# Optimization experiments

Measured on AMD Instinct MI355X. Metric: run time of the kernel, lower is better.

Reference implementation:

```python
import jax, jax.numpy as jnp
import numpy as np

B, IN_DIM, NUM_CLASS, OUT_CAPS, INIT_DIM, PCAP, T, LEAVES = 4096, 100, 4, 16, 64, 32, 16, 32
SUB = OUT_CAPS // NUM_CLASS          # 4
D = IN_DIM + INIT_DIM                # 164, digit_input_dim
M = PCAP + 1                         # 33 primary capsules
VBS = 256                            # GBN virtual batch size
EPS = 1e-5
DIN1 = T * SUB                       # 64, decoder input dim
DIN2 = DIN1 + 16                     # 80, after cat with conv1 out (base_outdim//2)


def entmax15(x, axis=-1):
    # exact alpha=1.5 entmax (Peters/Niculae/Martins), sort-based threshold
    x = jnp.moveaxis(x, axis, -1)
    x = (x - jnp.max(x, axis=-1, keepdims=True)) / 2.0
    d = x.shape[-1]
    xs = -jnp.sort(-x, axis=-1)  # descending
    rho = jnp.arange(1, d + 1, dtype=x.dtype)
    mean = jnp.cumsum(xs, axis=-1) / rho
    mean_sq = jnp.cumsum(xs * xs, axis=-1) / rho
    ss = rho * (mean_sq - mean * mean)
    delta_nz = jnp.clip((1.0 - ss) / rho, 0.0)
    tau = mean - jnp.sqrt(delta_nz)
    support = jnp.sum(tau <= xs, axis=-1, keepdims=True)
    tau_star = jnp.take_along_axis(tau, support - 1, axis=-1)
    out = jnp.clip(x - tau_star, 0.0) ** 2
    return jnp.moveaxis(out, -1, axis)


def layernorm(x, g, b):
    m = jnp.mean(x, axis=-1, keepdims=True)
    v = jnp.mean((x - m) ** 2, axis=-1, keepdims=True)
    return (x - m) / jnp.sqrt(v + EPS) * g + b


def gbn(x, g, b):
    # Ghost BatchNorm (training-mode batch stats per virtual batch of VBS)
    n = x.shape[0] // VBS
    xr = x.reshape(n, VBS, -1)
    m = jnp.mean(xr, axis=1, keepdims=True)
    v = jnp.mean((xr - m) ** 2, axis=1, keepdims=True)
    xr = (xr - m) / jnp.sqrt(v + EPS)
    return (xr * g + b).reshape(x.shape)


def abstract_layer(x, mask_w, fc_w, fc_b, bn_g, bn_b, out_dim):
    # mask_w: [P, Din], fc_w: [P, 2*out, Din] (grouped 1x1 conv), fc_b: [P, 2*out]
    mask = entmax15(mask_w, axis=-1)                      # [P, Din]
    mx = mask[None] * x[:, None, :]                       # [B, P, Din]
    h = jnp.einsum('bpd,pod->bpo', mx, fc_w) + fc_b       # [B, P, 2*out]
    bsz, p = h.shape[0], h.shape[1]
    h = gbn(h.reshape(bsz, -1), bn_g, bn_b).reshape(bsz, p, 2 * out_dim)
    # GLU-style gate per path, summed over paths
    return jnp.sum(jax.nn.relu(jax.nn.sigmoid(h[..., :out_dim]) * h[..., out_dim:]), axis=1)


def forward(x, y, init_w, init_b, enc_ln_g, enc_ln_b, prim_fc, route_w, thread,
            leaves, caps_ln_g, caps_ln_b, m1_w, fc1_w, fc1_b, bn1_g, bn1_b,
            m2_w, fc2_w, fc2_b, bn2_g, bn2_b, dec_w, dec_b):
    bsz = x.shape[0]
    # ---- CapsuleEncoder ----
    init_x = x @ init_w.T + init_b                        # [B, INIT_DIM]
    f = jnp.concatenate([x, init_x], axis=1)              # [B, D]
    caps = f[:, :, None] * prim_fc[None]                  # [B, D, PCAP]
    caps = jnp.concatenate([caps, f[:, :, None]], axis=-1)  # [B, D, M]
    caps = jnp.swapaxes(caps, -1, -2)                     # [B, M, D]
    caps = layernorm(caps, enc_ln_g, enc_ln_b)
    # ---- InferCapsule ----
    w = entmax15(route_w, axis=-2)                        # [M, N, D, T], entmax over D
    priors = jnp.einsum('bmd,mndt->bmnt', caps, w)        # [B, M, N, T]
    lh = leaves / jnp.maximum(jnp.linalg.norm(leaves, axis=-1, keepdims=True), 1e-12)
    votes = jax.nn.sigmoid(jnp.einsum('lt,bmnt->bmnl', lh, priors))  # [B, M, N, L]
    dis = jnp.mean((votes - jnp.mean(votes, axis=1, keepdims=True)) ** 2, axis=-1)  # [B, M, N]
    wgt = jax.nn.relu(thread ** 2 - dis)
    prob = jax.nn.softmax(wgt, axis=-2)                   # softmax over M
    hidden = layernorm(jnp.einsum('bmn,bmnt->bnt', prob, priors), caps_ln_g, caps_ln_b)  # [B, N, T]
    # ---- head (eval: no dropout) ----
    norms = jnp.sqrt(jnp.sum(hidden ** 2, axis=-1))       # [B, N]
    pred = jnp.sum(norms.reshape(bsz, NUM_CLASS, SUB), axis=-1)
    # ---- label-gated capsule selection ----
    yr = jnp.tile(y, (1, SUB)).reshape(bsz, SUB, NUM_CLASS)
    hsel = jnp.sum(hidden.reshape(bsz, SUB, NUM_CLASS, T) * yr[..., None], axis=2)
    hsel = hsel.reshape(bsz, DIN1)                        # [B, 64]
    # ---- decoder: CapsuleDecoder_BasicBlock + Linear ----
    out1 = abstract_layer(hsel, m1_w, fc1_w, fc1_b, bn1_g, bn1_b, 16)
    h2 = jnp.concatenate([hsel, out1], axis=-1)           # [B, 80]
    out2 = abstract_layer(h2, m2_w, fc2_w, fc2_b, bn2_g, bn2_b, 32)
    rec = out2 @ dec_w.T + dec_b                          # [B, IN_DIM]
    return pred, rec


def setup_inputs() -> dict:
    ks = jax.random.split(jax.random.key(0), 20)
    d = {}
    d['x'] = jax.random.normal(ks[0], (B, IN_DIM), jnp.float32)
    d['y'] = jax.nn.one_hot(jax.random.randint(ks[1], (B,), 0, NUM_CLASS), NUM_CLASS, dtype=jnp.float32)
    d['init_w'] = jax.random.normal(ks[2], (INIT_DIM, IN_DIM), jnp.float32) * 0.1
    d['init_b'] = jnp.zeros((INIT_DIM,), jnp.float32)
    d['enc_ln_g'] = jnp.ones((D,), jnp.float32)
    d['enc_ln_b'] = jnp.zeros((D,), jnp.float32)
    d['prim_fc'] = jax.random.normal(ks[3], (D, PCAP), jnp.float32)
    d['route_w'] = jax.random.normal(ks[4], (M, OUT_CAPS, D, T), jnp.float32)
    d['thread'] = jax.random.uniform(ks[5], (1, M, OUT_CAPS), jnp.float32)
    d['leaves'] = jax.random.uniform(ks[6], (LEAVES, T), jnp.float32)
    d['caps_ln_g'] = jnp.ones((T,), jnp.float32)
    d['caps_ln_b'] = jnp.zeros((T,), jnp.float32)
    d['m1_w'] = jax.random.uniform(ks[7], (3, DIN1), jnp.float32)
    d['fc1_w'] = jax.random.normal(ks[8], (3, 32, DIN1), jnp.float32) * 0.1
    d['fc1_b'] = jnp.zeros((3, 32), jnp.float32)
    d['bn1_g'] = jnp.ones((3 * 32,), jnp.float32)
    d['bn1_b'] = jnp.zeros((3 * 32,), jnp.float32)
    d['m2_w'] = jax.random.uniform(ks[9], (3, DIN2), jnp.float32)
    d['fc2_w'] = jax.random.normal(ks[10], (3, 64, DIN2), jnp.float32) * 0.1
    d['fc2_b'] = jnp.zeros((3, 64), jnp.float32)
    d['bn2_g'] = jnp.ones((3 * 64,), jnp.float32)
    d['bn2_b'] = jnp.zeros((3 * 64,), jnp.float32)
    d['dec_w'] = jax.random.normal(ks[11], (IN_DIM, 32), jnp.float32) * 0.1
    d['dec_b'] = jnp.zeros((IN_DIM,), jnp.float32)
    return d


def reference(x, y, init_w, init_b, enc_ln_g, enc_ln_b, prim_fc, route_w, thread,
              leaves, caps_ln_g, caps_ln_b, m1_w, fc1_w, fc1_b, bn1_g, bn1_b,
              m2_w, fc2_w, fc2_b, bn2_g, bn2_b, dec_w, dec_b):
    return forward(x, y, init_w, init_b, enc_ln_g, enc_ln_b, prim_fc, route_w, thread,
                   leaves, caps_ln_g, caps_ln_b, m1_w, fc1_w, fc1_b, bn1_g, bn1_b,
                   m2_w, fc2_w, fc2_b, bn2_g, bn2_b, dec_w, dec_b)
```

## Files before the change

### kernel.cpp

```cpp
#include <hip/hip_runtime.h>
#include <hip/hip_fp16.h>

#define BATCH 4096
#define NCLS  4
#define INDIM 100
#define INITD 64
#define DD    164
#define DDP   192
#define MM    33
#define TT    16
#define NOUT  16

typedef _Float16 f16;
typedef f16 f16x8 __attribute__((ext_vector_type(8)));
typedef float f32x4 __attribute__((ext_vector_type(4)));

__global__ __launch_bounds__(256) void k_pre(const float* __restrict__ route_w,
    const float* __restrict__ m1_w, const float* __restrict__ m2_w,
    const float* __restrict__ leaves,
    __half* __restrict__ w2t, float* __restrict__ mask1, float* __restrict__ mask2,
    float* __restrict__ lh_t){
  int blk = blockIdx.x, tid = threadIdx.x;
  if (blk < 528){
    const float* base = route_w + (size_t)blk*DD*16;
    int l  = tid & 63;
    int t  = (tid>>6)*4 + (l&3);
    int lg = l>>2;
    float v[11];
    float mx = -1e30f;
    #pragma unroll
    for (int i=0;i<11;++i){
      int d = lg + 16*i;
      v[i] = (d < DD) ? base[d*16 + t] : -1e30f;
      mx = fmaxf(mx, v[i]);
    }
    #pragma unroll
    for (int msk=4; msk<=32; msk<<=1) mx = fmaxf(mx, __shfl_xor(mx, msk));
    #pragma unroll
    for (int i=0;i<11;++i) v[i] = (v[i]-mx)*0.5f;
    float lo=-1.0f, hi=0.0f;
    for (int it=0; it<30; ++it){
      float mid = 0.5f*(lo+hi), g=0.0f;
      #pragma unroll
      for (int i=0;i<11;++i){ float tv = fmaxf(v[i]-mid, 0.0f); g += tv*tv; }
      #pragma unroll
      for (int msk=4; msk<=32; msk<<=1) g += __shfl_xor(g, msk);
      if (g > 1.0f) lo = mid; else hi = mid;
    }
    float tau = 0.5f*(lo+hi);
    __half* wout = w2t + (size_t)(blk*16 + t)*DDP;
    #pragma unroll
    for (int i=0;i<12;++i){
      int d = lg + 16*i;
      if (d < DDP){
        float tv = 0.0f;
        if (i < 11 && d < DD){ tv = fmaxf(v[i]-tau, 0.0f); }
        wout[d] = __float2half(tv*tv);
      }
    }
  } else if (blk == 528){
    int wv = tid>>6, l = tid&63;
    if (wv < 3){
      float v0 = m1_w[wv*64 + l];
      float mx = v0;
      #pragma unroll
      for (int m=1;m<=32;m<<=1) mx = fmaxf(mx, __shfl_xor(mx,m));
      v0 = (v0-mx)*0.5f;
      float lo=-1.0f, hi=0.0f;
      for (int it=0;it<30;++it){
        float mid = 0.5f*(lo+hi);
        float tv = fmaxf(v0-mid, 0.0f);
        float g = tv*tv;
        #pragma unroll
        for (int m=1;m<=32;m<<=1) g += __shfl_xor(g,m);
        if (g > 1.0f) lo = mid; else hi = mid;
      }
      float tau = 0.5f*(lo+hi);
      float tv = fmaxf(v0-tau, 0.0f);
      mask1[wv*64 + l] = tv*tv;
    } else if (l < 32){
      int li = l;
      float s=0.0f;
      for (int t=0;t<TT;++t){ float vv=leaves[li*TT+t]; s+=vv*vv; }
      float dn = fmaxf(sqrtf(s), 1e-12f);
      for (int t=0;t<TT;++t) lh_t[t*32+li] = leaves[li*TT+t]/dn;
    }
  } else {
    int wv = tid>>6, l = tid&63;
    if (wv < 3){
      float v0 = m2_w[wv*80 + l];
      float v1 = (l < 16) ? m2_w[wv*80 + 64 + l] : -1e30f;
      float mx = fmaxf(v0, v1);
      #pragma unroll
      for (int m=1;m<=32;m<<=1) mx = fmaxf(mx, __shfl_xor(mx,m));
      v0 = (v0-mx)*0.5f; v1 = (v1-mx)*0.5f;
      float lo=-1.0f, hi=0.0f;
      for (int it=0;it<30;++it){
        float mid = 0.5f*(lo+hi);
        float t0 = fmaxf(v0-mid, 0.0f), t1 = fmaxf(v1-mid, 0.0f);
        float g = t0*t0 + t1*t1;
        #pragma unroll
        for (int m=1;m<=32;m<<=1) g += __shfl_xor(g,m);
        if (g > 1.0f) lo = mid; else hi = mid;
      }
      float tau = 0.5f*(lo+hi);
      float t0 = fmaxf(v0-tau, 0.0f);
      mask2[wv*80 + l] = t0*t0;
      if (l < 16){ float t1 = fmaxf(v1-tau, 0.0f); mask2[wv*80 + 64 + l] = t1*t1; }
    }
  }
}

__global__ __launch_bounds__(256) void k_caps(const float* __restrict__ x,
    const float* __restrict__ init_w, const float* __restrict__ init_b,
    const float* __restrict__ ln_g, const float* __restrict__ ln_b,
    const float* __restrict__ prim_fc, __half* __restrict__ caps_t, int b0, int nrows){
  int bl = blockIdx.x, b = b0 + bl, tid = threadIdx.x;
  __shared__ float f[DD], gs[DD], bs[DD], pfs[DD*32];
  if (tid < INDIM) f[tid] = x[(size_t)b*INDIM + tid];
  if (tid < DD){ gs[tid] = ln_g[tid]; bs[tid] = ln_b[tid]; }
  for (int i = tid; i < DD*32; i += 256) pfs[i] = prim_fc[i];
  __syncthreads();
  if (tid < INITD){
    float s = init_b[tid];
    for (int k=0;k<INDIM;++k) s += f[k]*init_w[tid*INDIM+k];
    f[INDIM+tid] = s;
  }
  __syncthreads();
  int w = tid>>6, lane = tid&63;
  for (int mi = w; mi < MM; mi += 4){
    float c[3]; float sum=0.0f, sq=0.0f;
    #pragma unroll
    for (int j=0;j<3;++j){
      int d = lane + 64*j;
      float v = 0.0f;
      if (d < DD) v = (mi < 32) ? f[d]*pfs[d*32+mi] : f[d];
      c[j] = v; sum += v; sq += v*v;
    }
    #pragma unroll
    for (int off=32; off; off>>=1){ sum += __shfl_xor(sum,off); sq += __shfl_xor(sq,off); }
    float mean = sum*(1.0f/DD);
    float var  = fmaxf(sq*(1.0f/DD) - mean*mean, 0.0f);
    float rstd = rsqrtf(var + 1e-5f);
    #pragma unroll
    for (int j=0;j<3;++j){
      int d = lane + 64*j;
      float o = (d < DD) ? ((c[j]-mean)*rstd*gs[d] + bs[d]) : 0.0f;
      caps_t[((size_t)mi*nrows + bl)*DDP + d] = __float2half(o);
    }
  }
}

__global__ __launch_bounds__(256) void k_gemm_mfma(const f16* __restrict__ caps_t,
    const f16* __restrict__ w2t, __half* __restrict__ priors, int nrows){
  int m = blockIdx.y, b0 = blockIdx.x*64;
  int tid = threadIdx.x;
  int wave = tid>>6, lane = tid&63;
  __shared__ f16 Al[64][40];
  __shared__ f16 Wl[256][40];
  f32x4 acc[4][4];
  #pragma unroll
  for (int i=0;i<4;++i)
    #pragma unroll
    for (int j=0;j<4;++j) acc[i][j] = (f32x4){0.f,0.f,0.f,0.f};

  int ar = tid>>2, ac0 = (tid&3)*8;
  int rg = lane&15, kg = lane>>4;

  for (int kc = 0; kc < 6; ++kc){
    *(uint4*)&Al[ar][ac0] =
        *(const uint4*)&caps_t[((size_t)m*nrows + b0 + ar)*DDP + kc*32 + ac0];
    #pragma unroll
    for (int c=0;c<4;++c)
      *(uint4*)&Wl[tid][c*8] =
          *(const uint4*)&w2t[((size_t)m*256 + tid)*DDP + kc*32 + c*8];
    __syncthreads();
    f16x8 a[4], bf[4];
    #pragma unroll
    for (int i=0;i<4;++i) a[i]  = *(const f16x8*)&Al[i*16 + rg][kg*8];
    #pragma unroll
    for (int j=0;j<4;++j) bf[j] = *(const f16x8*)&Wl[wave*64 + j*16 + rg][kg*8];
    #pragma unroll
    for (int i=0;i<4;++i)
      #pragma unroll
      for (int j=0;j<4;++j)
        acc[i][j] = __builtin_amdgcn_mfma_f32_16x16x32_f16(a[i], bf[j], acc[i][j], 0, 0, 0);
    __syncthreads();
  }
  int rg4 = kg*4, cc = rg;
  #pragma unroll
  for (int i=0;i<4;++i)
    #pragma unroll
    for (int j=0;j<4;++j)
      #pragma unroll
      for (int r=0;r<4;++r)
        priors[(size_t)(b0 + i*16 + rg4 + r)*(MM*256) + m*256 + wave*64 + j*16 + cc]
            = __float2half(acc[i][j][r]);
}

__global__ __launch_bounds__(256) void k_route(const __half* __restrict__ priors,
    const float* __restrict__ lh_t, const float* __restrict__ thr_in,
    const float* __restrict__ cg, const float* __restrict__ cbv,
    const float* __restrict__ y, float* __restrict__ out_pred, float* __restrict__ hsel,
    int b0){
  int bl = blockIdx.x, b = b0 + bl, tid = threadIdx.x;
  __shared__ __half pr[MM*256];
  __shared__ float lhs[512];
  __shared__ float votesT[32][265];
  __shared__ float vmeanT[32][9];
  __shared__ float wp[8*MM];
  __shared__ float hid[16*16];
  __shared__ float nrm[16];
  __shared__ float yw[4];
  {
    const unsigned* pbw = (const unsigned*)(priors + (size_t)bl*(MM*256));
    unsigned* prw = (unsigned*)pr;
    for (int i = tid; i < (MM*256)/2; i += 256) prw[i] = pbw[i];
  }
  for (int i = tid; i < 512; i += 256) lhs[i] = lh_t[i];
  if (tid < 4) yw[tid] = y[(size_t)b*4 + tid];
  __syncthreads();

  for (int nc = 0; nc < 2; ++nc){
    int nl = tid >> 5, l = tid & 31, n = nc*8 + nl;
    {
      float lh_reg[TT];
      #pragma unroll
      for (int t=0;t<TT;++t) lh_reg[t] = lhs[t*32+l];
      float vsum = 0.0f;
      for (int m=0;m<MM;++m){
        float s = 0.0f;
        const __half* p0 = &pr[m*256 + n*16];
        #pragma unroll
        for (int t=0;t<TT;++t) s += lh_reg[t]*__half2float(p0[t]);
        float v = 1.0f/(1.0f+__expf(-s));
        votesT[l][nl*MM+m] = v;
        vsum += v;
      }
      vmeanT[l][nl] = vsum*(1.0f/MM);
    }
    __syncthreads();
    for (int i = tid; i < 8*MM; i += 256){
      int nl2 = i/MM, m = i%MM, n2 = nc*8 + nl2;
      float s = 0.0f;
      #pragma unroll 8
      for (int l2=0;l2<32;++l2){
        float dd = votesT[l2][i] - vmeanT[l2][nl2];
        s += dd*dd;
      }
      float dis = s*(1.0f/32);
      float th = thr_in[m*NOUT + n2];
      wp[nl2*MM+m] = fmaxf(th*th - dis, 0.0f);
    }
    __syncthreads();
    if (tid < 8){
      float mx = -1e30f;
      for (int m=0;m<MM;++m) mx = fmaxf(mx, wp[tid*MM+m]);
      float s = 0.0f;
      for (int m=0;m<MM;++m){ float e = __expf(wp[tid*MM+m]-mx); wp[tid*MM+m] = e; s += e; }
      float inv = 1.0f/s;
      for (int m=0;m<MM;++m) wp[tid*MM+m] *= inv;
    }
    __syncthreads();
    if (tid < 128){
      int nl3 = tid >> 4, t = tid & 15, n3 = nc*8 + nl3;
      float s = 0.0f;
      for (int m=0;m<MM;++m) s += wp[nl3*MM+m]*__half2float(pr[m*256 + n3*16 + t]);
      hid[n3*16+t] = s;
    }
    __syncthreads();
  }
  if (tid < 16){
    float s=0.0f, q=0.0f;
    for (int t=0;t<TT;++t){ float v=hid[tid*16+t]; s+=v; q+=v*v; }
    float mean = s*(1.0f/TT);
    float var  = fmaxf(q*(1.0f/TT)-mean*mean, 0.0f);
    float rstd = rsqrtf(var + 1e-5f);
    float nn = 0.0f;
    for (int t=0;t<TT;++t){
      float v = (hid[tid*16+t]-mean)*rstd*cg[t] + cbv[t];
      hid[tid*16+t] = v; nn += v*v;
    }
    nrm[tid] = sqrtf(nn);
  }
  __syncthreads();
  if (tid < 4)
    out_pred[(size_t)b*4 + tid] = nrm[tid*4+0]+nrm[tid*4+1]+nrm[tid*4+2]+nrm[tid*4+3];
  if (tid < 64){
    int s2 = tid >> 4, t = tid & 15;
    float v = 0.0f;
    #pragma unroll
    for (int c=0;c<4;++c) v += yw[c]*hid[(s2*4+c)*16 + t];
    hsel[(size_t)b*64 + tid] = v;
  }
}

__global__ __launch_bounds__(256) void k_h1(const float* __restrict__ hsel,
    const float* __restrict__ mask1, const float* __restrict__ fc1_w,
    const float* __restrict__ fc1_b, float* __restrict__ h1){
  int idx = blockIdx.x*256 + threadIdx.x;
  if (idx >= BATCH*96) return;
  int b = idx/96, j = idx%96, p = j>>5;
  float s = fc1_b[j];
  const float* hs = hsel + (size_t)b*64;
  const float* mk = mask1 + p*64;
  const float* wr = fc1_w + (size_t)j*64;
  for (int d=0; d<64; ++d) s += mk[d]*hs[d]*wr[d];
  h1[idx] = s;
}

__global__ __launch_bounds__(256) void k_stats(const float* __restrict__ h,
    float* __restrict__ stats, int F){
  int vb = blockIdx.x / F, j = blockIdx.x % F;
  float v = h[(size_t)(vb*256 + threadIdx.x)*F + j];
  float s = v, q = v*v;
  #pragma unroll
  for (int off=32; off; off>>=1){ s += __shfl_xor(s,off); q += __shfl_xor(q,off); }
  __shared__ float ps[4], pq[4];
  int w = threadIdx.x >> 6;
  if ((threadIdx.x & 63) == 0){ ps[w]=s; pq[w]=q; }
  __syncthreads();
  if (threadIdx.x == 0){
    float ss = ps[0]+ps[1]+ps[2]+ps[3];
    float qq = pq[0]+pq[1]+pq[2]+pq[3];
    float mean = ss*(1.0f/256);
    float var  = fmaxf(qq*(1.0f/256) - mean*mean, 0.0f);
    stats[(size_t)blockIdx.x*2]   = mean;
    stats[(size_t)blockIdx.x*2+1] = rsqrtf(var + 1e-5f);
  }
}

__global__ __launch_bounds__(192) void k_out1h2(const float* __restrict__ hsel,
    const float* __restrict__ h1, const float* __restrict__ stats1,
    const float* __restrict__ bn1g, const float* __restrict__ bn1b,
    const float* __restrict__ mask2, const float* __restrict__ fc2_w,
    const float* __restrict__ fc2_b, float* __restrict__ h2raw){
  int b = blockIdx.x, tid = threadIdx.x, vb = b >> 8;
  __shared__ float h2s[80];
  if (tid < 64) h2s[tid] = hsel[(size_t)b*64 + tid];
  if (tid < 16){
    float s = 0.0f;
    for (int p=0;p<3;++p){
      int ja = p*32 + tid, jb = ja + 16;
      float ha = (h1[(size_t)b*96+ja]-stats1[(vb*96+ja)*2])*stats1[(vb*96+ja)*2+1]*bn1g[ja] + bn1b[ja];
      float hb = (h1[(size_t)b*96+jb]-stats1[(vb*96+jb)*2])*stats1[(vb*96+jb)*2+1]*bn1g[jb] + bn1b[jb];
      float sg = 1.0f/(1.0f+__expf(-ha));
      s += fmaxf(sg*hb, 0.0f);
    }
    h2s[64+tid] = s;
  }
  __syncthreads();
  int p = tid >> 6;
  float s = fc2_b[tid];
  const float* mk = mask2 + p*80;
  const float* wr = fc2_w + (size_t)tid*80;
  for (int d=0; d<80; ++d) s += mk[d]*h2s[d]*wr[d];
  h2raw[(size_t)b*192 + tid] = s;
}

__global__ __launch_bounds__(128) void k_final(const float* __restrict__ h2raw,
    const float* __restrict__ stats2, const float* __restrict__ bn2g,
    const float* __restrict__ bn2b, const float* __restrict__ dec_w,
    const float* __restrict__ dec_b, float* __restrict__ out_rec){
  int b = blockIdx.x, tid = threadIdx.x, vb = b >> 8;
  __shared__ float o2[32];
  if (tid < 32){
    float s = 0.0f;
    for (int p=0;p<3;++p){
      int ja = p*64 + tid, jb = ja + 32;
      float ha = (h2raw[(size_t)b*192+ja]-stats2[(vb*192+ja)*2])*stats2[(vb*192+ja)*2+1]*bn2g[ja] + bn2b[ja];
      float hb = (h2raw[(size_t)b*192+jb]-stats2[(vb*192+jb)*2])*stats2[(vb*192+jb)*2+1]*bn2g[jb] + bn2b[jb];
      float sg = 1.0f/(1.0f+__expf(-ha));
      s += fmaxf(sg*hb, 0.0f);
    }
    o2[tid] = s;
  }
  __syncthreads();
  if (tid < INDIM){
    float r = dec_b[tid];
    #pragma unroll
    for (int o=0;o<32;++o) r += o2[o]*dec_w[tid*32+o];
    out_rec[(size_t)b*INDIM + tid] = r;
  }
}

extern "C" void kernel_launch(void* const* d_in, const int* in_sizes, int n_in,
                              void* d_out, int out_size, void* d_ws, size_t ws_size,
                              hipStream_t stream){
  const float* x      = (const float*)d_in[0];
  const float* y      = (const float*)d_in[1];
  const float* init_w = (const float*)d_in[2];
  const float* init_b = (const float*)d_in[3];
  const float* eg     = (const float*)d_in[4];
  const float* ebv    = (const float*)d_in[5];
  const float* pf     = (const float*)d_in[6];
  const float* rw     = (const float*)d_in[7];
  const float* thr    = (const float*)d_in[8];
  const float* lv     = (const float*)d_in[9];
  const float* cg     = (const float*)d_in[10];
  const float* cbv    = (const float*)d_in[11];
  const float* m1w    = (const float*)d_in[12];
  const float* f1w    = (const float*)d_in[13];
  const float* f1b    = (const float*)d_in[14];
  const float* g1     = (const float*)d_in[15];
  const float* b1     = (const float*)d_in[16];
  const float* m2w    = (const float*)d_in[17];
  const float* f2w    = (const float*)d_in[18];
  const float* f2b    = (const float*)d_in[19];
  const float* g2     = (const float*)d_in[20];
  const float* b2v    = (const float*)d_in[21];
  const float* dw     = (const float*)d_in[22];
  const float* db     = (const float*)d_in[23];
  char* ws = (char*)d_ws;
  float* out = (float*)d_out;
  (void)in_sizes; (void)n_in; (void)out_size;

  size_t offs[11];
  auto layout = [&](size_t nrows)->size_t{
    size_t o = 0; int i = 0;
    auto put = [&](size_t bytes){ offs[i++] = o; o = (o + bytes + 255) & ~(size_t)255; };
    put((size_t)MM*256*DDP*sizeof(__half));
    put((size_t)MM*nrows*DDP*sizeof(__half));
    put((size_t)nrows*MM*256*sizeof(__half));
    put(192*sizeof(float));
    put(240*sizeof(float));
    put(512*sizeof(float));
    put((size_t)BATCH*64*sizeof(float));
    put((size_t)BATCH*96*sizeof(float));
    put(16*96*2*sizeof(float));
    put((size_t)BATCH*192*sizeof(float));
    put(16*192*2*sizeof(float));
    return o;
  };
  int nrows = BATCH, nchunk = 1;
  if (layout(BATCH) > ws_size){ nrows = 1024; nchunk = 4; layout(1024); }
  __half* w2   = (__half*)(ws + offs[0]);
  __half* caps = (__half*)(ws + offs[1]);
  __half* pri  = (__half*)(ws + offs[2]);
  float*  m1   = (float*)(ws + offs[3]);
  float*  m2   = (float*)(ws + offs[4]);
  float*  lh   = (float*)(ws + offs[5]);
  float*  hsel = (float*)(ws + offs[6]);
  float*  h1   = (float*)(ws + offs[7]);
  float*  s1   = (float*)(ws + offs[8]);
  float*  h2   = (float*)(ws + offs[9]);
  float*  s2   = (float*)(ws + offs[10]);

  k_pre<<<dim3(530), dim3(256), 0, stream>>>(rw, m1w, m2w, lv, w2, m1, m2, lh);

  for (int c = 0; c < nchunk; ++c){
    int b0 = c*nrows;
    k_caps<<<dim3(nrows), dim3(256), 0, stream>>>(x, init_w, init_b, eg, ebv, pf,
        caps, b0, nrows);
    k_gemm_mfma<<<dim3(nrows/64, MM), dim3(256), 0, stream>>>(
        (const f16*)caps, (const f16*)w2, pri, nrows);
    k_route<<<dim3(nrows), dim3(256), 0, stream>>>(pri, lh, thr, cg, cbv, y,
        out, hsel, b0);
  }

  k_h1<<<dim3((BATCH*96)/256), dim3(256), 0, stream>>>(hsel, m1, f1w, f1b, h1);
  k_stats<<<dim3(16*96), dim3(256), 0, stream>>>(h1, s1, 96);
  k_out1h2<<<dim3(BATCH), dim3(192), 0, stream>>>(hsel, h1, s1, g1, b1,
      m2, f2w, f2b, h2);
  k_stats<<<dim3(16*192), dim3(256), 0, stream>>>(h2, s2, 192);
  k_final<<<dim3(BATCH), dim3(128), 0, stream>>>(h2, s2, g2, b2v, dw, db,
      out + (size_t)BATCH*NCLS);
}
```

Measured before the change: 468.6 us.

## Keep routing votes in registers and reduce with warp shuffles in k_route

Restructures the per-sample routing kernel so each thread holds its 33 sigmoid votes in registers. The variance across leaves is computed with xor-shuffles over the 32 lanes, and the softmax and weighted sum are done per lane instead of in serial thread subsets. This removes the large votesT shared buffer, several __syncthreads barriers per chunk, and the stages where only 8 or 128 threads were active. Priors are now read with 8-wide half vector loads. The cost is much higher register pressure (33 floats plus 16 lh values per thread), which could lower occupancy, and some redundant exp and softmax work across lanes.

New measurement: 414.3 us. 11.6% less time.

```diff
diff --git a/kernel.cpp b/kernel.cpp
--- a/kernel.cpp
+++ b/kernel.cpp
@@ -206,9 +206,7 @@
   int bl = blockIdx.x, b = b0 + bl, tid = threadIdx.x;
   __shared__ __half pr[MM*256];
   __shared__ float lhs[512];
-  __shared__ float votesT[32][265];
-  __shared__ float vmeanT[32][9];
-  __shared__ float wp[8*MM];
+  __shared__ float th2s[MM*16];
   __shared__ float hid[16*16];
   __shared__ float nrm[16];
   __shared__ float yw[4];
@@ -218,68 +216,70 @@
     for (int i = tid; i < (MM*256)/2; i += 256) prw[i] = pbw[i];
   }
   for (int i = tid; i < 512; i += 256) lhs[i] = lh_t[i];
+  for (int i = tid; i < MM*16; i += 256){ float t = thr_in[i]; th2s[i] = t*t; }
   if (tid < 4) yw[tid] = y[(size_t)b*4 + tid];
   __syncthreads();
 
+  int nl = tid >> 5, l = tid & 31;
+  float lh_reg[TT];
+  #pragma unroll
+  for (int t=0;t<TT;++t) lh_reg[t] = lhs[t*32+l];
+
   for (int nc = 0; nc < 2; ++nc){
-    int nl = tid >> 5, l = tid & 31, n = nc*8 + nl;
-    {
-      float lh_reg[TT];
-      #pragma unroll
-      for (int t=0;t<TT;++t) lh_reg[t] = lhs[t*32+l];
-      float vsum = 0.0f;
-      for (int m=0;m<MM;++m){
-        float s = 0.0f;
-        const __half* p0 = &pr[m*256 + n*16];
-        #pragma unroll
-        for (int t=0;t<TT;++t) s += lh_reg[t]*__half2float(p0[t]);
-        float v = 1.0f/(1.0f+__expf(-s));
-        votesT[l][nl*MM+m] = v;
-        vsum += v;
-      }
-      vmeanT[l][nl] = vsum*(1.0f/MM);
-    }
-    __syncthreads();
-    for (int i = tid; i < 8*MM; i += 256){
-      int nl2 = i/MM, m = i%MM, n2 = nc*8 + nl2;
+    int n = nc*8 + nl;
+    float v[MM];
+    float vsum = 0.0f;
+    #pragma unroll
+    for (int m=0;m<MM;++m){
+      const f16* p0 = (const f16*)&pr[m*256 + n*16];
+      f16x8 a0 = *(const f16x8*)p0;
+      f16x8 a1 = *(const f16x8*)(p0+8);
       float s = 0.0f;
-      #pragma unroll 8
-      for (int l2=0;l2<32;++l2){
-        float dd = votesT[l2][i] - vmeanT[l2][nl2];
-        s += dd*dd;
-      }
-      float dis = s*(1.0f/32);
-      float th = thr_in[m*NOUT + n2];
-      wp[nl2*MM+m] = fmaxf(th*th - dis, 0.0f);
-    }
-    __syncthreads();
-    if (tid < 8){
-      float mx = -1e30f;
-      for (int m=0;m<MM;++m) mx = fmaxf(mx, wp[tid*MM+m]);
-      float s = 0.0f;
-      for (int m=0;m<MM;++m){ float e = __expf(wp[tid*MM+m]-mx); wp[tid*MM+m] = e; s += e; }
-      float inv = 1.0f/s;
-      for (int m=0;m<MM;++m) wp[tid*MM+m] *= inv;
-    }
-    __syncthreads();
-    if (tid < 128){
-      int nl3 = tid >> 4, t = tid & 15, n3 = nc*8 + nl3;
-      float s = 0.0f;
-      for (int m=0;m<MM;++m) s += wp[nl3*MM+m]*__half2float(pr[m*256 + n3*16 + t]);
-      hid[n3*16+t] = s;
-    }
-    __syncthreads();
-  }
+      #pragma unroll
+      for (int t=0;t<8;++t) s += lh_reg[t]*(float)a0[t];
+      #pragma unroll
+      for (int t=0;t<8;++t) s += lh_reg[8+t]*(float)a1[t];
+      float vv = 1.0f/(1.0f+__expf(-s));
+      v[m] = vv; vsum += vv;
+    }
+    float mean_m = vsum*(1.0f/MM);
+    float mx = -1e30f;
+    #pragma unroll
+    for (int m=0;m<MM;++m){
+      float dd = v[m] - mean_m;
+      float sq = dd*dd;
+      #pragma unroll
+      for (int msk=1; msk<=16; msk<<=1) sq += __shfl_xor(sq, msk);
+      float wg = fmaxf(th2s[m*16+n] - sq*(1.0f/32), 0.0f);
+      v[m] = wg; mx = fmaxf(mx, wg);
+    }
+    float ssum = 0.0f;
+    #pragma unroll
+    for (int m=0;m<MM;++m){ float e = __expf(v[m]-mx); v[m] = e; ssum += e; }
+    float inv = 1.0f/ssum;
+    int t = l & 15;
+    float h = 0.0f;
+    if (l < 16){
+      #pragma unroll
+      for (int m=0;m<=16;++m) h += v[m]*(float)((const f16*)pr)[m*256 + n*16 + t];
+    } else {
+      #pragma unroll
+      for (int m=17;m<MM;++m) h += v[m]*(float)((const f16*)pr)[m*256 + n*16 + t];
+    }
+    h += __shfl_xor(h, 16);
+    if (l < 16) hid[n*16+t] = h*inv;
+  }
+  __syncthreads();
   if (tid < 16){
     float s=0.0f, q=0.0f;
-    for (int t=0;t<TT;++t){ float v=hid[tid*16+t]; s+=v; q+=v*v; }
+    for (int t=0;t<TT;++t){ float v2=hid[tid*16+t]; s+=v2; q+=v2*v2; }
     float mean = s*(1.0f/TT);
     float var  = fmaxf(q*(1.0f/TT)-mean*mean, 0.0f);
     float rstd = rsqrtf(var + 1e-5f);
     float nn = 0.0f;
     for (int t=0;t<TT;++t){
-      float v = (hid[tid*16+t]-mean)*rstd*cg[t] + cbv[t];
-      hid[tid*16+t] = v; nn += v*v;
+      float v2 = (hid[tid*16+t]-mean)*rstd*cg[t] + cbv[t];
+      hid[tid*16+t] = v2; nn += v2*v2;
     }
     nrm[tid] = sqrtf(nn);
   }
@@ -288,10 +288,10 @@
     out_pred[(size_t)b*4 + tid] = nrm[tid*4+0]+nrm[tid*4+1]+nrm[tid*4+2]+nrm[tid*4+3];
   if (tid < 64){
     int s2 = tid >> 4, t = tid & 15;
-    float v = 0.0f;
-    #pragma unroll
-    for (int c=0;c<4;++c) v += yw[c]*hid[(s2*4+c)*16 + t];
-    hsel[(size_t)b*64 + tid] = v;
+    float v2 = 0.0f;
+    #pragma unroll
+    for (int c=0;c<4;++c) v2 += yw[c]*hid[(s2*4+c)*16 + t];
+    hsel[(size_t)b*64 + tid] = v2;
   }
 }
 
```
